# Kernel tuning notes

Hardware: AMD Instinct MI355X
Metric: run time of the kernel (lower is better)

The kernel has to match this reference:

```python
import jax, jax.numpy as jnp
import numpy as np

GAMMA = 0.1
PENALTY = 0.0
BANDWIDTH = 1.0e6
B, N, M = 64, 512, 512


def setup_inputs() -> dict:
    key = jax.random.key(0)
    k1, k2, k3 = jax.random.split(key, 3)
    D = jax.random.uniform(k1, (B, N, M), dtype=jnp.float32)
    mask = jnp.ones((B, N, M), dtype=jnp.float32)
    # valid lengths in [N/2, N] so R[b, x_lens[b], y_lens[b]] is always reachable
    x_lens = jax.random.randint(k2, (B,), N // 2, N + 1)
    y_lens = jax.random.randint(k3, (B,), M // 2, M + 1)
    return {"D": D, "mask": mask, "x_lens": x_lens, "y_lens": y_lens}


def _softdtw(D, x_lens, y_lens):
    # Soft-DTW DP over anti-diagonals. D: [B, N, M] masked cost.
    # Returns per-batch loss R[b, x_lens[b], y_lens[b]].
    Bn, Nn, Mn = D.shape
    inv_gamma = 1.0 / GAMMA
    inf = jnp.float32(jnp.inf)
    ii = jnp.arange(Nn + 1)  # row index i = 0..N within a diagonal buffer
    im1 = jnp.clip(ii - 1, 0, Nn)
    # diagonal buffers: entry i of diag s holds R[i, s - i]
    d0 = jnp.full((Bn, Nn + 1), inf).at[:, 0].set(0.0)  # s=0: only R[0,0]=0
    d1 = jnp.full((Bn, Nn + 1), inf)                    # s=1: boundary, all inf
    xl = x_lens[:, None]
    yl = y_lens[:, None]

    def step(carry, s):
        dm2, dm1 = carry                      # diagonals s-2 and s-1
        jj = s - ii                           # column index j for each i
        r00 = dm2[:, im1]                     # R[i-1, j-1]
        r01 = dm1[:, im1]                     # R[i-1, j]
        r10 = dm1                             # R[i,   j-1]
        r0 = -r00 * inv_gamma
        r1 = -(r01 + PENALTY) * inv_gamma
        r2 = -(r10 + PENALTY) * inv_gamma
        rmax = jnp.maximum(jnp.maximum(r0, r1), r2)
        finite = jnp.isfinite(rmax)
        rs = jnp.where(finite, rmax, 0.0)     # safe max (avoid inf-inf -> nan)
        rsum = jnp.exp(r0 - rs) + jnp.exp(r1 - rs) + jnp.exp(r2 - rs)
        softmin = jnp.where(finite, -GAMMA * (jnp.log(rsum) + rs), inf)
        dcell = D[:, jnp.clip(ii - 1, 0, Nn - 1), jnp.clip(jj - 1, 0, Mn - 1)]
        new = dcell + softmin                 # R[i, j] = D[i-1, j-1] + softmin
        valid = (ii >= 1) & (ii <= Nn) & (jj >= 1) & (jj <= Mn)
        valid = valid & (jnp.abs(jj - ii) <= BANDWIDTH)
        upd = valid[None, :] & (ii[None, :] <= xl) & (jj[None, :] <= yl)
        dnew = jnp.where(upd, new, inf)
        return (dm1, dnew), dnew

    _, diags = jax.lax.scan(step, (d0, d1), jnp.arange(2, Nn + Mn + 1))
    # diags: [N+M-1, B, N+1]; diag index s-2 holds cells with i+j == s
    s_idx = jnp.clip(x_lens + y_lens - 2, 0, Nn + Mn - 2)
    loss = diags[s_idx, jnp.arange(Bn), x_lens]
    return loss


def reference(D, mask, x_lens, y_lens):
    return _softdtw(D * mask, x_lens, y_lens)
```

## Files before the change

kernel.cpp:

```cpp
#include <hip/hip_runtime.h>


constexpr int Bn = 64, Nn = 512, Mn = 512;
constexpr int TARGET_E = -30;

__device__ __forceinline__ float exp2_fast(float x) {
    float r; asm("v_exp_f32 %0, %1" : "=v"(r) : "v"(x)); return r;
}
__device__ __forceinline__ float log2_fast(float x) {
    float r; asm("v_log_f32 %0, %1" : "=v"(r) : "v"(x)); return r;
}
__device__ __forceinline__ float ldexp_fast(float x, int e) {
    float r; asm("v_ldexp_f32 %0, %1, %2" : "=v"(r) : "v"(x), "v"(e)); return r;
}
__device__ __forceinline__ int frexp_exp(float x) {
    int r; asm("v_frexp_exp_i32_f32 %0, %1" : "=v"(r) : "v"(x)); return r;
}

#define LOADROWS(MM, BD, BM)                                                   \
    {   const int base_ = 4 * ((MM) - t);                                      \
        _Pragma("unroll")                                                      \
        for (int rr = 0; rr < 4; ++rr) {                                       \
            int r_ = min(max(base_ + rr, 0), Nn - 1);                          \
            int o_ = r_ * (Mn / 4) + chunk;                                    \
            BD[rr][0] = D4[o_];  BD[rr][1] = D4[o_ + 1];                       \
            BM[rr][0] = M4[o_];  BM[rr][1] = M4[o_ + 1];                       \
        } }

#define BUILDW(BD, BM)                                                         \
    {   _Pragma("unroll")                                                      \
        for (int rr = 0; rr < 4; ++rr) {                                       \
            float4 p_ = BD[rr][0] * BM[rr][0] * negk;                          \
            float4 q_ = BD[rr][1] * BM[rr][1] * negk;                          \
            W[rr][0] = exp2_fast(p_.x); W[rr][1] = exp2_fast(p_.y);            \
            W[rr][2] = exp2_fast(p_.z); W[rr][3] = exp2_fast(p_.w);            \
            W[rr][4] = exp2_fast(q_.x); W[rr][5] = exp2_fast(q_.y);            \
            W[rr][6] = exp2_fast(q_.z); W[rr][7] = exp2_fast(q_.w);            \
        } }

#define STEP(MM, BI_D, BI_M, BW_D, BW_M)                                       \
    {                                                                          \
        LOADROWS((MM) + 2, BI_D, BI_M);                                        \
        if ((MM) == t && t != 0) {                                             \
            _Pragma("unroll")                                                  \
            for (int c = 0; c < 8; ++c) E[c] = 0.0f;                           \
            Ld = 0.0f;                                                         \
        }                                                                      \
        float ce[4], co[4];                                                    \
        _Pragma("unroll")                                                      \
        for (int rr = 0; rr < 4; ++rr) {                                       \
            float c0_ = (rr == 0) ? Ld : L[rr - 1];                            \
            float c2_ = L[rr];                                                 \
            float A_[8], Bv_[8];                                               \
            A_[0] = E[0] + c0_;                                                \
            _Pragma("unroll")                                                  \
            for (int c = 1; c < 8; ++c) A_[c] = E[c] + E[c - 1];               \
            _Pragma("unroll")                                                  \
            for (int c = 0; c < 8; ++c) Bv_[c] = W[rr][c] * A_[c];             \
            _Pragma("unroll")                                                  \
            for (int c = 0; c < 8; ++c) {                                      \
                float nv_ = fmaf(W[rr][c], c2_, Bv_[c]);                       \
                E[c] = nv_;  c2_ = nv_;                                        \
            }                                                                  \
            ce[rr] = c2_;  co[rr] = __shfl_up(c2_, 1);                         \
            if ((MM) == m_out && rr == r_out) {             \
                float sel_ = E[0];                                             \
                if (c_out == 1) sel_ = E[1];  if (c_out == 2) sel_ = E[2];     \
                if (c_out == 3) sel_ = E[3];  if (c_out == 4) sel_ = E[4];     \
                if (c_out == 5) sel_ = E[5];  if (c_out == 6) sel_ = E[6];     \
                if (c_out == 7) sel_ = E[7];                                   \
                ov = sel_;  ovS = S;                                           \
            }                                                                  \
        }                                                                      \
        int So_ = __shfl_up(S, 1);                                             \
        int eo_ = frexp_exp(ce[3]);                                            \
        int ei_ = frexp_exp(co[3]) + (So_ - S);                                \
        bool own0_  = (ce[3] == 0.0f);                                         \
        bool incok_ = (t != 0) && (co[3] != 0.0f);                             \
        int  eref_  = (incok_ && ((ei_ > eo_) || own0_)) ? ei_ : eo_;          \
        int  shift_ = (own0_ && !incok_) ? 0 : (TARGET_E - eref_);             \
        if ((MM) < t) shift_ = S - So_;              \
        int Snew_ = S - shift_;                                                \
        _Pragma("unroll")                                                      \
        for (int c = 0; c < 8; ++c) E[c] = ldexp_fast(E[c], shift_);           \
        Ld = ldexp_fast(L[3], shift_);                                         \
        {   int d_ = So_ - Snew_;                                              \
            _Pragma("unroll")                                                  \
            for (int rr = 0; rr < 4; ++rr)                                     \
                L[rr] = (t == 0) ? 0.0f : ldexp_fast(co[rr], d_);              \
        }                                                                      \
        S = Snew_;                                                             \
        BUILDW(BW_D, BW_M);                                                    \
    }

__global__ __launch_bounds__(64) void softdtw_fwd(
    const float* __restrict__ D, const float* __restrict__ Msk,
    const int* __restrict__ xlens, const int* __restrict__ ylens,
    float* __restrict__ out)
{
    const int b = blockIdx.x;
    const int t = threadIdx.x;
    const int xl = xlens[b];
    const int yl = ylens[b];
    const int t_out = (yl - 1) >> 3;
    const int c_out = (yl - 1) & 7;
    const int r_out = (xl - 1) & 3;
    const int m_out = ((xl - 1) >> 2) + t_out;

    const float negk = -14.4269504088896341f;
    const float klog = 0.06931471805599453f;

    const float4* __restrict__ D4 = (const float4*)(D   + (size_t)b * (Nn * Mn));
    const float4* __restrict__ M4 = (const float4*)(Msk + (size_t)b * (Nn * Mn));
    const int chunk = t * 2;

    float E[8];
#pragma unroll
    for (int c = 0; c < 8; ++c) E[c] = 0.0f;
    float L[4] = {0.0f, 0.0f, 0.0f, 0.0f};
    float Ld = (t == 0) ? 1.0f : 0.0f;
    int S = 0;
    float ov = 1.0f;  int ovS = 0;

    float W[4][8];
    float4 bAD[4][2], bAM[4][2];
    float4 bBD[4][2], bBM[4][2];

    LOADROWS(0, bAD, bAM);
    BUILDW(bAD, bAM);
    LOADROWS(1, bBD, bBM);

    int m = 0;
    for (; m + 1 <= m_out; m += 2) {
        STEP(m,     bAD, bAM, bBD, bBM);
        STEP(m + 1, bBD, bBM, bAD, bAM);
    }
    if (m <= m_out) STEP(m, bAD, bAM, bBD, bBM);

    if (t == t_out) {
        int   ev = frexp_exp(ov);
        float mv = ldexp_fast(ov, -ev);
        out[b] = -(log2_fast(mv) + (float)(ev + ovS)) * klog;
    }
}

extern "C" void kernel_launch(void* const* d_in, const int* in_sizes, int n_in,
                              void* d_out, int out_size, void* d_ws, size_t ws_size,
                              hipStream_t stream) {
    const float* D   = (const float*)d_in[0];
    const float* Msk = (const float*)d_in[1];
    const int*   xl  = (const int*)d_in[2];
    const int*   yl  = (const int*)d_in[3];
    float* out = (float*)d_out;
    softdtw_fwd<<<dim3(Bn), dim3(64), 0, stream>>>(D, Msk, xl, yl, out);
}
```

Measured before the change: 145.9 us.

## Warp-specialize: producer wavefronts build exp weights into LDS ring for compute wave

```diff
diff --git a/kernel.cpp b/kernel.cpp
--- a/kernel.cpp
+++ b/kernel.cpp
@@ -17,53 +17,69 @@
     int r; asm("v_frexp_exp_i32_f32 %0, %1" : "=v"(r) : "v"(x)); return r;
 }
 
-#define LOADROWS(MM, BD, BM)                                                   \
+#define PLOAD(MM)                                                              \
     {   const int base_ = 4 * ((MM) - t);                                      \
         _Pragma("unroll")                                                      \
         for (int rr = 0; rr < 4; ++rr) {                                       \
             int r_ = min(max(base_ + rr, 0), Nn - 1);                          \
             int o_ = r_ * (Mn / 4) + chunk;                                    \
-            BD[rr][0] = D4[o_];  BD[rr][1] = D4[o_ + 1];                       \
-            BM[rr][0] = M4[o_];  BM[rr][1] = M4[o_ + 1];                       \
+            pD[rr][0] = D4[o_];  pD[rr][1] = D4[o_ + 1];                       \
+            pM[rr][0] = M4[o_];  pM[rr][1] = M4[o_ + 1];                       \
         } }
 
-#define BUILDW(BD, BM)                                                         \
-    {   _Pragma("unroll")                                                      \
+#define PBUILD(MM)                                                             \
+    {   const int s_ = (MM) % 6;                                               \
+        _Pragma("unroll")                                                      \
         for (int rr = 0; rr < 4; ++rr) {                                       \
-            float4 p_ = BD[rr][0] * BM[rr][0] * negk;                          \
-            float4 q_ = BD[rr][1] * BM[rr][1] * negk;                          \
-            W[rr][0] = exp2_fast(p_.x); W[rr][1] = exp2_fast(p_.y);            \
-            W[rr][2] = exp2_fast(p_.z); W[rr][3] = exp2_fast(p_.w);            \
-            W[rr][4] = exp2_fast(q_.x); W[rr][5] = exp2_fast(q_.y);            \
-            W[rr][6] = exp2_fast(q_.z); W[rr][7] = exp2_fast(q_.w);            \
+            float4 p_ = pD[rr][0] * pM[rr][0] * negk;                          \
+            float4 q_ = pD[rr][1] * pM[rr][1] * negk;                          \
+            float4 wa_, wb_;                                                   \
+            wa_.x = exp2_fast(p_.x);  wa_.y = exp2_fast(p_.y);                 \
+            wa_.z = exp2_fast(p_.z);  wa_.w = exp2_fast(p_.w);                 \
+            wb_.x = exp2_fast(q_.x);  wb_.y = exp2_fast(q_.y);                 \
+            wb_.z = exp2_fast(q_.z);  wb_.w = exp2_fast(q_.w);                 \
+            wlds[s_][2 * rr][t]     = wa_;                                     \
+            wlds[s_][2 * rr + 1][t] = wb_;                                     \
         } }
 
-#define STEP(MM, BI_D, BI_M, BW_D, BW_M)                                       \
+#define CSTEP(MM, WCUR, WNXT)                                                  \
     {                                                                          \
-        LOADROWS((MM) + 2, BI_D, BI_M);                                        \
-        if ((MM) == t && t != 0) {                                             \
+        const int m_ = (MM);                                                   \
+        {   const int sn_ = (m_ + 1) % 6;                                      \
             _Pragma("unroll")                                                  \
-            for (int c = 0; c < 8; ++c) E[c] = 0.0f;                           \
-            Ld = 0.0f;                                                         \
+            for (int rr = 0; rr < 4; ++rr) {                                   \
+                WNXT[rr][0] = wlds[sn_][2 * rr][t];                            \
+                WNXT[rr][1] = wlds[sn_][2 * rr + 1][t];                        \
+            } }                                                                \
+        if (m_ <= 63) {                                   \
+            if (m_ == t && t != 0) {                                           \
+                _Pragma("unroll")                                              \
+                for (int c = 0; c < 8; ++c) E[c] = 0.0f;                       \
+                Ld = 0.0f;                                                     \
+            }                                                                  \
         }                                                                      \
-        float ce[4], co[4];                                                    \
+        float ce3_, co_[4];                                                    \
         _Pragma("unroll")                                                      \
         for (int rr = 0; rr < 4; ++rr) {                                       \
-            float c0_ = (rr == 0) ? Ld : L[rr - 1];                            \
+            const float Wr_[8] = {                                             \
+                WCUR[rr][0].x, WCUR[rr][0].y, WCUR[rr][0].z, WCUR[rr][0].w,    \
+                WCUR[rr][1].x, WCUR[rr][1].y, WCUR[rr][1].z, WCUR[rr][1].w };  \
+            const float c0s_ = (rr == 0) ? Ld : L[rr - 1];                     \
             float c2_ = L[rr];                                                 \
             float A_[8], Bv_[8];                                               \
-            A_[0] = E[0] + c0_;                                                \
+            A_[0] = E[0] + c0s_;                                               \
             _Pragma("unroll")                                                  \
             for (int c = 1; c < 8; ++c) A_[c] = E[c] + E[c - 1];               \
             _Pragma("unroll")                                                  \
-            for (int c = 0; c < 8; ++c) Bv_[c] = W[rr][c] * A_[c];             \
+            for (int c = 0; c < 8; ++c) Bv_[c] = Wr_[c] * A_[c];               \
             _Pragma("unroll")                                                  \
             for (int c = 0; c < 8; ++c) {                                      \
-                float nv_ = fmaf(W[rr][c], c2_, Bv_[c]);                       \
+                float nv_ = fmaf(Wr_[c], c2_, Bv_[c]);                         \
                 E[c] = nv_;  c2_ = nv_;                                        \
             }                                                                  \
-            ce[rr] = c2_;  co[rr] = __shfl_up(c2_, 1);                         \
-            if ((MM) == m_out && rr == r_out) {             \
+            if (rr == 3) ce3_ = c2_;                                           \
+            co_[rr] = __shfl_up(c2_, 1);                                       \
+            if (m_ == m_out && rr == r_out) {         \
                 float sel_ = E[0];                                             \
                 if (c_out == 1) sel_ = E[1];  if (c_out == 2) sel_ = E[2];     \
                 if (c_out == 3) sel_ = E[3];  if (c_out == 4) sel_ = E[4];     \
@@ -73,13 +89,13 @@
             }                                                                  \
         }                                                                      \
         int So_ = __shfl_up(S, 1);                                             \
-        int eo_ = frexp_exp(ce[3]);                                            \
-        int ei_ = frexp_exp(co[3]) + (So_ - S);                                \
-        bool own0_  = (ce[3] == 0.0f);                                         \
-        bool incok_ = (t != 0) && (co[3] != 0.0f);                             \
+        int eo_ = frexp_exp(ce3_);                                             \
+        int ei_ = frexp_exp(co_[3]) + (So_ - S);                               \
+        bool own0_  = (ce3_ == 0.0f);                                          \
+        bool incok_ = (t != 0) && (co_[3] != 0.0f);                            \
         int  eref_  = (incok_ && ((ei_ > eo_) || own0_)) ? ei_ : eo_;          \
         int  shift_ = (own0_ && !incok_) ? 0 : (TARGET_E - eref_);             \
-        if ((MM) < t) shift_ = S - So_;              \
+        if (m_ < t) shift_ = S - So_;                \
         int Snew_ = S - shift_;                                                \
         _Pragma("unroll")                                                      \
         for (int c = 0; c < 8; ++c) E[c] = ldexp_fast(E[c], shift_);           \
@@ -87,28 +103,32 @@
         {   int d_ = So_ - Snew_;                                              \
             _Pragma("unroll")                                                  \
             for (int rr = 0; rr < 4; ++rr)                                     \
-                L[rr] = (t == 0) ? 0.0f : ldexp_fast(co[rr], d_);              \
+                L[rr] = (t == 0) ? 0.0f : ldexp_fast(co_[rr], d_);             \
         }                                                                      \
         S = Snew_;                                                             \
-        BUILDW(BW_D, BW_M);                                                    \
     }
 
-__global__ __launch_bounds__(64) void softdtw_fwd(
+__global__ __launch_bounds__(192) void softdtw_fwd(
     const float* __restrict__ D, const float* __restrict__ Msk,
     const int* __restrict__ xlens, const int* __restrict__ ylens,
     float* __restrict__ out)
 {
-    const int b = blockIdx.x;
-    const int t = threadIdx.x;
+    const int tid = threadIdx.x;
+    const int w   = tid >> 6;
+    const int t   = tid & 63;
+    const int b   = blockIdx.x;
     const int xl = xlens[b];
     const int yl = ylens[b];
     const int t_out = (yl - 1) >> 3;
     const int c_out = (yl - 1) & 7;
     const int r_out = (xl - 1) & 3;
     const int m_out = ((xl - 1) >> 2) + t_out;
+    const int nsuper = (m_out >> 1) + 1;
 
     const float negk = -14.4269504088896341f;
     const float klog = 0.06931471805599453f;
+
+    __shared__ float4 wlds[6][8][64];
 
     const float4* __restrict__ D4 = (const float4*)(D   + (size_t)b * (Nn * Mn));
     const float4* __restrict__ M4 = (const float4*)(Msk + (size_t)b * (Nn * Mn));
@@ -121,23 +141,43 @@
     float Ld = (t == 0) ? 1.0f : 0.0f;
     int S = 0;
     float ov = 1.0f;  int ovS = 0;
+    float4 Wc[4][2], Wn[4][2];
 
-    float W[4][8];
-    float4 bAD[4][2], bAM[4][2];
-    float4 bBD[4][2], bBM[4][2];
+    float4 pD[4][2], pM[4][2];
 
-    LOADROWS(0, bAD, bAM);
-    BUILDW(bAD, bAM);
-    LOADROWS(1, bBD, bBM);
+    if (w == 1) {
+        PLOAD(0); PBUILD(0);
+        PLOAD(2); PBUILD(2);
+        PLOAD(4);
+    } else if (w == 2) {
+        PLOAD(1); PBUILD(1);
+        PLOAD(3); PBUILD(3);
+        PLOAD(5);
+    }
+    __syncthreads();
+    if (w == 0) {
+#pragma unroll
+        for (int rr = 0; rr < 4; ++rr) {
+            Wc[rr][0] = wlds[0][2 * rr][t];
+            Wc[rr][1] = wlds[0][2 * rr + 1][t];
+        }
+    }
 
-    int m = 0;
-    for (; m + 1 <= m_out; m += 2) {
-        STEP(m,     bAD, bAM, bBD, bBM);
-        STEP(m + 1, bBD, bBM, bAD, bAM);
+    for (int u = 0; u < nsuper; ++u) {
+        if (w == 0) {
+            CSTEP(2 * u, Wc, Wn);
+            if (2 * u + 1 <= m_out) CSTEP(2 * u + 1, Wn, Wc);
+        } else if (w == 1) {
+            PBUILD(2 * u + 4);
+            PLOAD(2 * u + 6);
+        } else {
+            PBUILD(2 * u + 5);
+            PLOAD(2 * u + 7);
+        }
+        __syncthreads();
     }
-    if (m <= m_out) STEP(m, bAD, bAM, bBD, bBM);
 
-    if (t == t_out) {
+    if (w == 0 && t == t_out) {
         int   ev = frexp_exp(ov);
         float mv = ldexp_fast(ov, -ev);
         out[b] = -(log2_fast(mv) + (float)(ev + ovS)) * klog;
@@ -152,5 +192,5 @@
     const int*   xl  = (const int*)d_in[2];
     const int*   yl  = (const int*)d_in[3];
     float* out = (float*)d_out;
-    softdtw_fwd<<<dim3(Bn), dim3(64), 0, stream>>>(D, Msk, xl, yl, out);
+    softdtw_fwd<<<dim3(Bn), dim3(192), 0, stream>>>(D, Msk, xl, yl, out);
 }
```

Measured after the change: 145.7 us. About the same (-0.2%).
